# Performance work log

Hardware: AMD Instinct MI355X
Metric: run time of the kernel (lower is better)

The kernel has to match this reference:

```python
import jax, jax.numpy as jnp
import numpy as np

B, M, D, H, DH = 4, 2048, 1024, 16, 64
R_ATTN, FFN_D, R_FFN = 32, 4096, 512
ROPE_THETA = 10000.0
LN_EPS = 1e-5


def layernorm(x, w, b):
    mu = jnp.mean(x, axis=-1, keepdims=True)
    var = jnp.mean(jnp.square(x - mu), axis=-1, keepdims=True)
    return (x - mu) * jax.lax.rsqrt(var + LN_EPS) * w + b


def headwise_svd(x, U, V, b):
    # x: [B,M,D]; U: [H,D,r]; V: [H,r,dh] -> [B,M,H,dh]
    xr = jnp.einsum('bmd,hdr->bmhr', x, U)
    y = jnp.einsum('bmhr,hrk->bmhk', xr, V)
    return y + b.reshape(U.shape[0], -1)


def rotate_half(x):
    x1, x2 = jnp.split(x, 2, axis=-1)
    return jnp.concatenate([-x2, x1], axis=-1)


def rope_cos_sin(m, dh, dtype):
    inv_freq = 1.0 / (ROPE_THETA ** (jnp.arange(0, dh, 2, dtype=jnp.float32) / dh))
    freqs = jnp.arange(m, dtype=jnp.float32)[:, None] * inv_freq[None, :]  # [M, dh/2]
    emb = jnp.concatenate([freqs, freqs], axis=-1)  # [M, dh]
    return jnp.cos(emb).astype(dtype), jnp.sin(emb).astype(dtype)


def setup_inputs() -> dict:
    key = jax.random.key(0)
    ks = jax.random.split(key, 16)
    s = 0.02
    def n(k, shape, scale=s):
        return jax.random.normal(k, shape, dtype=jnp.float32) * scale
    return dict(
        hidden_states=jax.random.normal(ks[0], (B, M, D), dtype=jnp.float32),
        attention_mask=jnp.ones((B, M), dtype=jnp.int32),
        ln1_w=jnp.ones((D,), jnp.float32), ln1_b=jnp.zeros((D,), jnp.float32),
        Uq=n(ks[1], (H, D, R_ATTN)), Vq=n(ks[2], (H, R_ATTN, DH)), bq=jnp.zeros((D,), jnp.float32),
        Uk=n(ks[3], (H, D, R_ATTN)), Vk=n(ks[4], (H, R_ATTN, DH)), bk=jnp.zeros((D,), jnp.float32),
        Uv=n(ks[5], (H, D, R_ATTN)), Vv=n(ks[6], (H, R_ATTN, DH)), bv=jnp.zeros((D,), jnp.float32),
        Wo_attn=n(ks[7], (D, D)), bo_attn=jnp.zeros((D,), jnp.float32),
        ln2_w=jnp.ones((D,), jnp.float32), ln2_b=jnp.zeros((D,), jnp.float32),
        U_wi=n(ks[8], (D, R_FFN)), V_wi=n(ks[9], (R_FFN, 2 * FFN_D)), b_wi=jnp.zeros((2 * FFN_D,), jnp.float32),
        U_wo=n(ks[10], (FFN_D, R_FFN)), V_wo=n(ks[11], (R_FFN, D)), b_wo=jnp.zeros((D,), jnp.float32),
    )


def reference(hidden_states, attention_mask, ln1_w, ln1_b,
              Uq, Vq, bq, Uk, Vk, bk, Uv, Vv, bv,
              Wo_attn, bo_attn, ln2_w, ln2_b,
              U_wi, V_wi, b_wi, U_wo, V_wo, b_wo):
    x = hidden_states
    xn = layernorm(x, ln1_w, ln1_b)

    # head-wise low-rank SVD QKV projections -> [B,H,M,dh]
    q = headwise_svd(xn, Uq, Vq, bq).transpose(0, 2, 1, 3)
    k = headwise_svd(xn, Uk, Vk, bk).transpose(0, 2, 1, 3)
    v = headwise_svd(xn, Uv, Vv, bv).transpose(0, 2, 1, 3)

    cos, sin = rope_cos_sin(x.shape[1], q.shape[-1], q.dtype)  # [M, dh], broadcasts
    q = q * cos + rotate_half(q) * sin
    k = k * cos + rotate_half(k) * sin

    scale = 1.0 / jnp.sqrt(jnp.asarray(q.shape[-1], q.dtype))
    scores = jnp.einsum('bhqd,bhkd->bhqk', q, k) * scale
    pad = (attention_mask == 0)[:, None, None, :]  # [B,1,1,M]
    scores = jnp.where(pad, jnp.finfo(scores.dtype).min, scores)
    attn = jax.nn.softmax(scores, axis=-1)
    ctx = jnp.einsum('bhqk,bhkd->bhqd', attn, v)
    ctx = ctx.transpose(0, 2, 1, 3).reshape(x.shape)  # [B,M,D]
    attn_out = jnp.einsum('bmd,ed->bme', ctx, Wo_attn) + bo_attn  # dense Wo (torch Linear)
    x = x + attn_out

    # FFN: low-rank Wi -> GEGLU(tanh) -> low-rank Wo
    xn2 = layernorm(x, ln2_w, ln2_b)
    h = (xn2 @ U_wi) @ V_wi + b_wi  # [B,M,2*FFN_D]
    h1, h2 = jnp.split(h, 2, axis=-1)
    g = jax.nn.gelu(h1, approximate=True) * h2  # GEGLU, tanh approx
    ffn_out = (g @ U_wo) @ V_wo + b_wo
    return x + ffn_out
```

## Files before the change

kernel.cpp:

```cpp
#include <hip/hip_runtime.h>
#include <cstdint>

#define DEV __device__ __forceinline__

typedef __attribute__((ext_vector_type(8))) short bf16x8;
typedef __attribute__((ext_vector_type(4))) float f32x4;
typedef __attribute__((ext_vector_type(16))) float f32x16;

#define MFMA(a,b,c) __builtin_amdgcn_mfma_f32_16x16x32_bf16((a),(b),(c),0,0,0)
#define MFMA32(a,b,c) __builtin_amdgcn_mfma_f32_32x32x16_bf16((a),(b),(c),0,0,0)

DEV unsigned short f2bf(float f) {
  union { float f; unsigned u; } v; v.f = f;
  unsigned r = v.u + 0x7fffu + ((v.u >> 16) & 1u);
  return (unsigned short)(r >> 16);
}
DEV float bf2f(unsigned short s) {
  union { unsigned u; float f; } v; v.u = ((unsigned)s) << 16; return v.f;
}
DEV float max3f(float a, float b, float c) { return fmaxf(fmaxf(a, b), c); }

DEV void gload16(const unsigned short* g, short* l) {
  __builtin_amdgcn_global_load_lds(
      (const __attribute__((address_space(1))) unsigned*)g,
      (__attribute__((address_space(3))) unsigned*)l, 16, 0, 0);
}


__global__ void k_build_ut(const float* __restrict__ Uq, const float* __restrict__ Uk,
                           const float* __restrict__ Uv, unsigned short* __restrict__ Ut) {
  __shared__ float tile[32][33];
  int s = blockIdx.y;
  int proj = s >> 4, h = s & 15;
  const float* U = (proj == 0) ? Uq : (proj == 1) ? Uk : Uv;
  const float* Us = U + (size_t)h * 1024 * 32;
  int d0 = blockIdx.x * 32;
  int tx = threadIdx.x, ty = threadIdx.y;
#pragma unroll
  for (int i = ty; i < 32; i += 8)
    tile[i][tx] = Us[(size_t)(d0 + i) * 32 + tx];
  __syncthreads();
#pragma unroll
  for (int i = ty; i < 32; i += 8)
    Ut[(size_t)(s * 32 + i) * 1024 + d0 + tx] = f2bf(tile[tx][i]);
}

__global__ void k_build_vt(const float* __restrict__ Vq, const float* __restrict__ Vk,
                           const float* __restrict__ Vv, unsigned short* __restrict__ Vt) {
  int ph = blockIdx.x;
  int proj = ph >> 4, h = ph & 15;
  const float* V = (proj == 0) ? Vq : (proj == 1) ? Vk : Vv;
  const float* Vs = V + (size_t)h * 2048;
  int t = threadIdx.x;
#pragma unroll
  for (int idx = t; idx < 2048; idx += 256) {
    int dh = idx >> 5, r = idx & 31;
    Vt[(size_t)ph * 2048 + idx] = f2bf(Vs[r * 64 + dh]);
  }
}

__global__ void k_f2bf(const float* __restrict__ in, unsigned short* __restrict__ out, int n) {
  int i = blockIdx.x * 256 + threadIdx.x;
  if (i < n) out[i] = f2bf(in[i]);
}

__global__ void k_transpose_bf16(const float* __restrict__ in, unsigned short* __restrict__ out,
                                 int R, int C) {
  __shared__ float tile[32][33];
  int c0 = blockIdx.x * 32, r0 = blockIdx.y * 32;
  int tx = threadIdx.x, ty = threadIdx.y;
#pragma unroll
  for (int i = ty; i < 32; i += 8)
    tile[i][tx] = in[(size_t)(r0 + i) * C + c0 + tx];
  __syncthreads();
#pragma unroll
  for (int i = ty; i < 32; i += 8)
    out[(size_t)(c0 + i) * R + r0 + tx] = f2bf(tile[tx][i]);
}

__global__ __launch_bounds__(256) void k_vtrans(const unsigned short* __restrict__ qkv,
                                                unsigned short* __restrict__ vT) {
  __shared__ short t[64][66];
  int bh = blockIdx.y, b = bh >> 4, h = bh & 15;
  int m0 = blockIdx.x << 6;
  int tid = threadIdx.x;
  int rr = tid >> 2, cc = (tid & 3) << 4;
  const unsigned short* src = qkv + ((size_t)(b * 2048 + m0 + rr)) * 3072 + 2048 + h * 64 + cc;
  *(bf16x8*)&t[rr][cc] = *(const bf16x8*)src;
  *(bf16x8*)&t[rr][cc + 8] = *(const bf16x8*)(src + 8);
  __syncthreads();
  unsigned short* dst = vT + ((size_t)bh * 64 + rr) * 2048 + m0 + cc;
  bf16x8 o0, o1;
#pragma unroll
  for (int j = 0; j < 8; ++j) o0[j] = t[cc + j][rr];
#pragma unroll
  for (int j = 0; j < 8; ++j) o1[j] = t[cc + 8 + j][rr];
  *(bf16x8*)dst = o0;
  *(bf16x8*)(dst + 8) = o1;
}

__global__ __launch_bounds__(256) void k_layernorm(const float* __restrict__ x,
                                                   const float* __restrict__ w,
                                                   const float* __restrict__ b,
                                                   unsigned short* __restrict__ out) {
  int row = blockIdx.x;
  int tid = threadIdx.x;
  int lane = tid & 63, wid = tid >> 6;
  const float4 v = ((const float4*)(x + (size_t)row * 1024))[tid];
  float s = v.x + v.y + v.z + v.w;
  float s2 = v.x * v.x + v.y * v.y + v.z * v.z + v.w * v.w;
#pragma unroll
  for (int o = 1; o < 64; o <<= 1) { s += __shfl_xor(s, o); s2 += __shfl_xor(s2, o); }
  __shared__ float as_[4], as2_[4];
  if (lane == 0) { as_[wid] = s; as2_[wid] = s2; }
  __syncthreads();
  s = as_[0] + as_[1] + as_[2] + as_[3];
  s2 = as2_[0] + as2_[1] + as2_[2] + as2_[3];
  float mean = s * (1.f / 1024.f);
  float var = s2 * (1.f / 1024.f) - mean * mean;
  float inv = rsqrtf(var + 1e-5f);
  const float4 wv = ((const float4*)w)[tid];
  const float4 bv = ((const float4*)b)[tid];
  union { unsigned short u[4]; unsigned long long ll; } o;
  o.u[0] = f2bf((v.x - mean) * inv * wv.x + bv.x);
  o.u[1] = f2bf((v.y - mean) * inv * wv.y + bv.y);
  o.u[2] = f2bf((v.z - mean) * inv * wv.z + bv.z);
  o.u[3] = f2bf((v.w - mean) * inv * wv.w + bv.w);
  ((unsigned long long*)(out + (size_t)row * 1024))[tid] = o.ll;
}

template <int EPI>
__global__ __launch_bounds__(256, 2) void k_gemm(const unsigned short* __restrict__ A,
                                                 const unsigned short* __restrict__ Bt,
                                                 const float* __restrict__ bias,
                                                 const float* __restrict__ resid,
                                                 void* __restrict__ outp, int N, int K) {
  __shared__ short Al[128 * 32];
  __shared__ short Bl[128 * 32];
  int tid = threadIdx.x, lane = tid & 63, wid = tid >> 6;
  int wr = wid >> 1, wc = wid & 1;
  size_t row0 = (size_t)blockIdx.y * 128;
  int col0 = blockIdx.x * 128;
  int arow = lane >> 2, acol = (lane & 3) << 3;
  const unsigned short* Ag = A + (row0 + wid * 32 + arow) * K + acol;
  const unsigned short* Bg = Bt + ((size_t)(col0 + wid * 32 + arow)) * K + acol;
  short* Ald = Al + wid * 1024;
  short* Bld = Bl + wid * 1024;
  f32x4 acc[4][4] = {};
  int fr = lane & 15, fk = (lane >> 4) << 3;
  for (int k0 = 0; k0 < K; k0 += 32) {
    __syncthreads();
    gload16(Ag + k0, Ald);
    gload16(Ag + (size_t)16 * K + k0, Ald + 512);
    gload16(Bg + k0, Bld);
    gload16(Bg + (size_t)16 * K + k0, Bld + 512);
    __syncthreads();
    bf16x8 af[4], bfr[4];
#pragma unroll
    for (int i = 0; i < 4; ++i) {
      af[i] = *(const bf16x8*)&Al[(wr * 64 + i * 16 + fr) * 32 + fk];
      bfr[i] = *(const bf16x8*)&Bl[(wc * 64 + i * 16 + fr) * 32 + fk];
    }
#pragma unroll
    for (int i = 0; i < 4; ++i)
#pragma unroll
      for (int j = 0; j < 4; ++j) acc[i][j] = MFMA(af[i], bfr[j], acc[i][j]);
  }
  int cr = (lane >> 4) << 2, cc = lane & 15;
#pragma unroll
  for (int j = 0; j < 4; ++j) {
    int col = col0 + wc * 64 + j * 16 + cc;
    float bb = (EPI >= 1) ? bias[col] : 0.f;
#pragma unroll
    for (int i = 0; i < 4; ++i) {
#pragma unroll
      for (int r = 0; r < 4; ++r) {
        size_t row = row0 + wr * 64 + i * 16 + cr + r;
        float v = acc[i][j][r] + bb;
        if (EPI == 2)
          ((float*)outp)[row * N + col] = v + resid[row * N + col];
        else
          ((unsigned short*)outp)[row * N + col] = f2bf(v);
      }
    }
  }
}

__global__ __launch_bounds__(256, 2) void k_qkv(const unsigned short* __restrict__ A,
                                                const unsigned short* __restrict__ Ut,
                                                const unsigned short* __restrict__ Vt,
                                                const float* __restrict__ bq,
                                                const float* __restrict__ bk,
                                                const float* __restrict__ bv,
                                                unsigned short* __restrict__ qkv) {
  __shared__ short Al[128 * 32];
  __shared__ short Bl[128 * 32];
  __shared__ short Xr[4][64 * 72];
  const int K = 1024, N3 = 3072;
  int tid = threadIdx.x, lane = tid & 63, wid = tid >> 6;
  int wr = wid >> 1, wc = wid & 1;
  size_t row0 = (size_t)blockIdx.y * 128;
  int col0 = blockIdx.x * 128;
  int arow = lane >> 2, acol = (lane & 3) << 3;
  const unsigned short* Ag = A + (row0 + wid * 32 + arow) * K + acol;
  const unsigned short* Bg = Ut + ((size_t)(col0 + wid * 32 + arow)) * K + acol;
  short* Ald = Al + wid * 1024;
  short* Bld = Bl + wid * 1024;
  f32x4 acc[4][4] = {};
  int fr = lane & 15, fk = (lane >> 4) << 3;
  for (int k0 = 0; k0 < K; k0 += 32) {
    __syncthreads();
    gload16(Ag + k0, Ald);
    gload16(Ag + (size_t)16 * K + k0, Ald + 512);
    gload16(Bg + k0, Bld);
    gload16(Bg + (size_t)16 * K + k0, Bld + 512);
    __syncthreads();
    bf16x8 af[4], bfr[4];
#pragma unroll
    for (int i = 0; i < 4; ++i) {
      af[i] = *(const bf16x8*)&Al[(wr * 64 + i * 16 + fr) * 32 + fk];
      bfr[i] = *(const bf16x8*)&Bl[(wc * 64 + i * 16 + fr) * 32 + fk];
    }
#pragma unroll
    for (int i = 0; i < 4; ++i)
#pragma unroll
      for (int j = 0; j < 4; ++j) acc[i][j] = MFMA(af[i], bfr[j], acc[i][j]);
  }
  int cr = (lane >> 4) << 2, cc = lane & 15;
  short* xw = &Xr[wid][0];
#pragma unroll
  for (int j = 0; j < 4; ++j)
#pragma unroll
    for (int i = 0; i < 4; ++i)
#pragma unroll
      for (int r = 0; r < 4; ++r)
        xw[(i * 16 + cr + r) * 72 + j * 16 + cc] = (short)f2bf(acc[i][j][r]);
  int phbase = blockIdx.x * 4 + wc * 2;
  const f32x4 zero4 = {0.f, 0.f, 0.f, 0.f};
#pragma unroll
  for (int h2 = 0; h2 < 2; ++h2) {
    int ph = phbase + h2;
    int proj = ph >> 4, hh = ph & 15;
    bf16x8 af2[4], bf2[4];
#pragma unroll
    for (int i2 = 0; i2 < 4; ++i2)
      af2[i2] = *(const bf16x8*)&xw[(i2 * 16 + fr) * 72 + h2 * 32 + fk];
#pragma unroll
    for (int j2 = 0; j2 < 4; ++j2)
      bf2[j2] = *(const bf16x8*)(Vt + ((size_t)ph * 64 + j2 * 16 + fr) * 32 + fk);
    f32x4 a2[4][4];
#pragma unroll
    for (int i2 = 0; i2 < 4; ++i2)
#pragma unroll
      for (int j2 = 0; j2 < 4; ++j2) a2[i2][j2] = MFMA(af2[i2], bf2[j2], zero4);
    const float* bp = (proj == 0) ? bq : (proj == 1) ? bk : bv;
    int obase = proj * 1024 + hh * 64;
    if (proj == 2) {
#pragma unroll
      for (int j2 = 0; j2 < 4; ++j2) {
        int dh = j2 * 16 + cc;
        float bb = bp[hh * 64 + dh];
#pragma unroll
        for (int i2 = 0; i2 < 4; ++i2)
#pragma unroll
          for (int r = 0; r < 4; ++r) {
            size_t row = row0 + wr * 64 + i2 * 16 + cr + r;
            qkv[row * N3 + obase + dh] = f2bf(a2[i2][j2][r] + bb);
          }
      }
    } else {
      float sc = (proj == 0) ? 0.18033688011112042f : 1.f;
#pragma unroll
      for (int j2 = 0; j2 < 2; ++j2) {
        int irot = j2 * 16 + cc;
        float freq = __expf((float)irot * -0.28782313662425575f);
        float bb1 = bp[hh * 64 + irot];
        float bb2 = bp[hh * 64 + irot + 32];
#pragma unroll
        for (int i2 = 0; i2 < 4; ++i2)
#pragma unroll
          for (int r = 0; r < 4; ++r) {
            size_t row = row0 + wr * 64 + i2 * 16 + cr + r;
            int m = (int)(row & 2047);
            float x1v = a2[i2][j2][r] + bb1;
            float x2v = a2[i2][j2 + 2][r] + bb2;
            float sn, csn;
            __sincosf((float)m * freq, &sn, &csn);
            qkv[row * N3 + obase + irot] = f2bf((x1v * csn - x2v * sn) * sc);
            qkv[row * N3 + obase + irot + 32] = f2bf((x2v * csn + x1v * sn) * sc);
          }
      }
    }
  }
}

__global__ __launch_bounds__(256, 2) void k_gemm_geglu(const unsigned short* __restrict__ A,
                                                       const unsigned short* __restrict__ Bt,
                                                       const float* __restrict__ bias,
                                                       unsigned short* __restrict__ out) {
  __shared__ short Al[128 * 32];
  __shared__ short B1l[128 * 32];
  __shared__ short B2l[128 * 32];
  const int K = 512;
  int tid = threadIdx.x, lane = tid & 63, wid = tid >> 6;
  int wr = wid >> 1, wc = wid & 1;
  size_t row0 = (size_t)blockIdx.y * 128;
  int col0 = blockIdx.x * 128;
  int arow = lane >> 2, acol = (lane & 3) << 3;
  const unsigned short* Ag = A + (row0 + wid * 32 + arow) * K + acol;
  const unsigned short* B1g = Bt + ((size_t)(col0 + wid * 32 + arow)) * K + acol;
  const unsigned short* B2g = Bt + ((size_t)(col0 + 4096 + wid * 32 + arow)) * K + acol;
  short* Ald = Al + wid * 1024;
  short* B1d = B1l + wid * 1024;
  short* B2d = B2l + wid * 1024;
  f32x4 acc1[4][4] = {}, acc2[4][4] = {};
  int fr = lane & 15, fk = (lane >> 4) << 3;
  for (int k0 = 0; k0 < K; k0 += 32) {
    __syncthreads();
    gload16(Ag + k0, Ald);
    gload16(Ag + (size_t)16 * K + k0, Ald + 512);
    gload16(B1g + k0, B1d);
    gload16(B1g + (size_t)16 * K + k0, B1d + 512);
    gload16(B2g + k0, B2d);
    gload16(B2g + (size_t)16 * K + k0, B2d + 512);
    __syncthreads();
    bf16x8 af[4], b1f[4], b2f[4];
#pragma unroll
    for (int i = 0; i < 4; ++i) {
      af[i] = *(const bf16x8*)&Al[(wr * 64 + i * 16 + fr) * 32 + fk];
      b1f[i] = *(const bf16x8*)&B1l[(wc * 64 + i * 16 + fr) * 32 + fk];
      b2f[i] = *(const bf16x8*)&B2l[(wc * 64 + i * 16 + fr) * 32 + fk];
    }
#pragma unroll
    for (int i = 0; i < 4; ++i)
#pragma unroll
      for (int j = 0; j < 4; ++j) {
        acc1[i][j] = MFMA(af[i], b1f[j], acc1[i][j]);
        acc2[i][j] = MFMA(af[i], b2f[j], acc2[i][j]);
      }
  }
  int cr = (lane >> 4) << 2, cc = lane & 15;
#pragma unroll
  for (int j = 0; j < 4; ++j) {
    int col = col0 + wc * 64 + j * 16 + cc;
    float bb1 = bias[col], bb2 = bias[col + 4096];
#pragma unroll
    for (int i = 0; i < 4; ++i) {
#pragma unroll
      for (int r = 0; r < 4; ++r) {
        size_t row = row0 + wr * 64 + i * 16 + cr + r;
        float h1 = acc1[i][j][r] + bb1;
        float h2 = acc2[i][j][r] + bb2;
        float u = 0.7978845608028654f * (h1 + 0.044715f * h1 * h1 * h1);
        float e = __expf(2.f * u);
        float th = 1.f - 2.f / (e + 1.f);
        float gv = 0.5f * h1 * (1.f + th) * h2;
        out[row * 4096 + col] = f2bf(gv);
      }
    }
  }
}

#define KIX(r, c) ((r) * 64 + ((c) ^ (((r) & 7) << 3)))

__global__ __launch_bounds__(256, 4) void k_attn(const unsigned short* __restrict__ qkv,
                                                 const unsigned short* __restrict__ vT,
                                                 const int* __restrict__ mask,
                                                 unsigned short* __restrict__ ctx) {
  __shared__ short Kl[64 * 64];
  __shared__ short Vl[64 * 64];
  __shared__ short Ol[4][32 * 64];
  __shared__ float mpen[64];
  __shared__ int mflag;
  int bh = blockIdx.y, b = bh >> 4, h = bh & 15;
  int q0 = blockIdx.x << 7;
  int tid = threadIdx.x, lane = tid & 63, wid = tid >> 6;
  int qi = lane & 31, hi = lane >> 5;
  const unsigned short* qrow =
      qkv + ((size_t)(b * 2048 + q0 + wid * 32 + qi)) * 3072 + h * 64 + hi * 8;
  bf16x8 qa[4];
#pragma unroll
  for (int c = 0; c < 4; ++c) qa[c] = *(const bf16x8*)(qrow + c * 16);
  float m_r = -1e30f, l_r = 0.f;
  f32x16 oacc0 = {}, oacc1 = {};
  int srw = lane >> 3;
  int schx = ((lane & 7) ^ srw) << 3;
  int rb = wid * 16;
  const unsigned short* kgb =
      qkv + ((size_t)(b * 2048 + rb + srw)) * 3072 + 1024 + h * 64 + schx;
  const unsigned short* vgb = vT + ((size_t)(bh * 64 + rb + srw)) * 2048 + schx;
  short* kld = Kl + rb * 64;
  short* vld = Vl + rb * 64;
  const int* mbase = mask + b * 2048;
  const f32x16 zero16 = {};
  int mv = (tid < 64) ? mbase[tid] : 1;
  for (int k0 = 0; k0 < 2048; k0 += 64) {
    __syncthreads();
    gload16(kgb + (size_t)k0 * 3072, kld);
    gload16(kgb + (size_t)(k0 + 8) * 3072, kld + 512);
    gload16(vgb + k0, vld);
    gload16(vgb + (size_t)8 * 2048 + k0, vld + 512);
    if (wid == 0) {
      mpen[lane] = (mv == 0) ? -1e30f : 0.f;
      unsigned long long bal = __ballot(mv == 0);
      if (lane == 0) mflag = (bal != 0ull) ? 1 : 0;
    }
    if (k0 + 64 < 2048) mv = (tid < 64) ? mbase[k0 + 64 + tid] : 1;
    __syncthreads();
#pragma unroll
    for (int kt = 0; kt < 2; ++kt) {
      f32x16 s = zero16;
      __builtin_amdgcn_s_setprio(1);
#pragma unroll
      for (int c = 0; c < 4; ++c) {
        bf16x8 kf = *(const bf16x8*)&Kl[KIX(kt * 32 + qi, c * 16 + hi * 8)];
        s = MFMA32(kf, qa[c], s);
      }
      __builtin_amdgcn_s_setprio(0);
      if (mflag) {
        const f32x4* mp4 = (const f32x4*)mpen;
#pragma unroll
        for (int t = 0; t < 4; ++t) {
          f32x4 pen = mp4[kt * 8 + t * 2 + hi];
#pragma unroll
          for (int r = 0; r < 4; ++r) s[t * 4 + r] += pen[r];
        }
      }
      float t0 = max3f(s[0], s[1], s[2]);
      float t1 = max3f(s[3], s[4], s[5]);
      float t2 = max3f(s[6], s[7], s[8]);
      float t3 = max3f(s[9], s[10], s[11]);
      float t4 = max3f(s[12], s[13], s[14]);
      float t5 = fmaxf(t0, s[15]);
      float pmax = max3f(max3f(t5, t1, t2), t3, t4);
      pmax = fmaxf(pmax, __shfl_xor(pmax, 32));
      if (!__all(pmax - m_r <= 8.f)) {
        float mn = fmaxf(m_r, pmax);
        float fac = exp2f(m_r - mn);
        m_r = mn;
        l_r *= fac;
#pragma unroll
        for (int r = 0; r < 16; ++r) { oacc0[r] *= fac; oacc1[r] *= fac; }
      }
#pragma unroll
      for (int r = 0; r < 16; ++r) s[r] = exp2f(s[r] - m_r);
      float su0 = (s[0] + s[1]) + (s[2] + s[3]);
      float su1 = (s[4] + s[5]) + (s[6] + s[7]);
      float su2 = (s[8] + s[9]) + (s[10] + s[11]);
      float su3 = (s[12] + s[13]) + (s[14] + s[15]);
      l_r += (su0 + su1) + (su2 + su3);
      unsigned pk[8];
#pragma unroll
      for (int w = 0; w < 8; ++w)
        asm("v_cvt_pk_bf16_f32 %0, %1, %2" : "=v"(pk[w]) : "v"(s[2 * w]), "v"(s[2 * w + 1]));
      unsigned a0 = pk[0], b0 = pk[2];
      unsigned a1 = pk[1], b1 = pk[3];
      unsigned a2 = pk[4], b2 = pk[6];
      unsigned a3 = pk[5], b3 = pk[7];
      asm("v_permlane32_swap_b32 %0, %1" : "+v"(a0), "+v"(b0));
      asm("v_permlane32_swap_b32 %0, %1" : "+v"(a1), "+v"(b1));
      asm("v_permlane32_swap_b32 %0, %1" : "+v"(a2), "+v"(b2));
      asm("v_permlane32_swap_b32 %0, %1" : "+v"(a3), "+v"(b3));
      union { unsigned u[4]; bf16x8 v; } pb0, pb1;
      pb0.u[0] = a0; pb0.u[1] = a1; pb0.u[2] = b0; pb0.u[3] = b1;
      pb1.u[0] = a2; pb1.u[1] = a3; pb1.u[2] = b2; pb1.u[3] = b3;
      __builtin_amdgcn_s_setprio(1);
      {
        bf16x8 vf00 = *(const bf16x8*)&Vl[KIX(qi, kt * 32 + hi * 8)];
        bf16x8 vf01 = *(const bf16x8*)&Vl[KIX(qi, kt * 32 + 16 + hi * 8)];
        oacc0 = MFMA32(vf00, pb0.v, oacc0);
        oacc0 = MFMA32(vf01, pb1.v, oacc0);
        bf16x8 vf10 = *(const bf16x8*)&Vl[KIX(32 + qi, kt * 32 + hi * 8)];
        bf16x8 vf11 = *(const bf16x8*)&Vl[KIX(32 + qi, kt * 32 + 16 + hi * 8)];
        oacc1 = MFMA32(vf10, pb0.v, oacc1);
        oacc1 = MFMA32(vf11, pb1.v, oacc1);
      }
      __builtin_amdgcn_s_setprio(0);
    }
  }
  l_r += __shfl_xor(l_r, 32);
  float invl = 1.f / l_r;
  short* ob = &Ol[wid][0];
  int xsw = (qi & 7) << 3;
#pragma unroll
  for (int t = 0; t < 4; ++t) {
    int d = t * 8 + 4 * hi;
    float a0 = oacc0[4 * t] * invl, a1 = oacc0[4 * t + 1] * invl;
    float a2 = oacc0[4 * t + 2] * invl, a3 = oacc0[4 * t + 3] * invl;
    unsigned w0, w1;
    asm("v_cvt_pk_bf16_f32 %0, %1, %2" : "=v"(w0) : "v"(a0), "v"(a1));
    asm("v_cvt_pk_bf16_f32 %0, %1, %2" : "=v"(w1) : "v"(a2), "v"(a3));
    *(unsigned long long*)&ob[qi * 64 + (d ^ xsw)] =
        ((unsigned long long)w1 << 32) | (unsigned long long)w0;
    float c0 = oacc1[4 * t] * invl, c1 = oacc1[4 * t + 1] * invl;
    float c2 = oacc1[4 * t + 2] * invl, c3 = oacc1[4 * t + 3] * invl;
    unsigned w2, w3;
    asm("v_cvt_pk_bf16_f32 %0, %1, %2" : "=v"(w2) : "v"(c0), "v"(c1));
    asm("v_cvt_pk_bf16_f32 %0, %1, %2" : "=v"(w3) : "v"(c2), "v"(c3));
    *(unsigned long long*)&ob[qi * 64 + ((d + 32) ^ xsw)] =
        ((unsigned long long)w3 << 32) | (unsigned long long)w2;
  }
  __syncthreads();
#pragma unroll
  for (int p = 0; p < 2; ++p) {
    int q = p * 16 + (lane >> 2);
    int qx = (q & 7) << 3;
    unsigned short* dst =
        ctx + ((size_t)(b * 2048 + q0 + wid * 32 + q)) * 1024 + h * 64;
#pragma unroll
    for (int j = 0; j < 2; ++j) {
      int c = (lane & 3) * 8 + j * 32;
      bf16x8 vv = *(const bf16x8*)&ob[q * 64 + (c ^ qx)];
      __builtin_nontemporal_store(vv, (bf16x8*)(dst + c));
    }
  }
}

extern "C" void kernel_launch(void* const* d_in, const int* in_sizes, int n_in, void* d_out,
                              int out_size, void* d_ws, size_t ws_size, hipStream_t stream) {
  const float* x = (const float*)d_in[0];
  const int* amask = (const int*)d_in[1];
  const float* ln1w = (const float*)d_in[2];
  const float* ln1b = (const float*)d_in[3];
  const float* Uq = (const float*)d_in[4];
  const float* Vq = (const float*)d_in[5];
  const float* bq = (const float*)d_in[6];
  const float* Uk = (const float*)d_in[7];
  const float* Vk = (const float*)d_in[8];
  const float* bk = (const float*)d_in[9];
  const float* Uv = (const float*)d_in[10];
  const float* Vv = (const float*)d_in[11];
  const float* bv = (const float*)d_in[12];
  const float* Wo = (const float*)d_in[13];
  const float* bo = (const float*)d_in[14];
  const float* ln2w = (const float*)d_in[15];
  const float* ln2b = (const float*)d_in[16];
  const float* Uwi = (const float*)d_in[17];
  const float* Vwi = (const float*)d_in[18];
  const float* bwi = (const float*)d_in[19];
  const float* Uwo = (const float*)d_in[20];
  const float* Vwo = (const float*)d_in[21];
  const float* bwo = (const float*)d_in[22];

  char* ws = (char*)d_ws;
  size_t off = 0;
  auto alloc = [&](size_t bytes) {
    void* p = ws + off;
    off += (bytes + 255) & ~(size_t)255;
    return p;
  };
  unsigned short* xn = (unsigned short*)alloc((size_t)8192 * 1024 * 2);
  unsigned short* Ut = (unsigned short*)alloc((size_t)1536 * 1024 * 2);
  unsigned short* Vt = (unsigned short*)alloc((size_t)48 * 2048 * 2);
  unsigned short* Wob = (unsigned short*)alloc((size_t)1024 * 1024 * 2);
  unsigned short* Uwit = (unsigned short*)alloc((size_t)512 * 1024 * 2);
  unsigned short* Vwit = (unsigned short*)alloc((size_t)8192 * 512 * 2);
  unsigned short* Uwot = (unsigned short*)alloc((size_t)512 * 4096 * 2);
  unsigned short* Vwot = (unsigned short*)alloc((size_t)1024 * 512 * 2);
  unsigned short* qkv = (unsigned short*)alloc((size_t)8192 * 3072 * 2);
  unsigned short* ctx = (unsigned short*)alloc((size_t)8192 * 1024 * 2);
  float* x1 = (float*)alloc((size_t)8192 * 1024 * 4);
  unsigned short* hr = (unsigned short*)alloc((size_t)8192 * 512 * 2);
  unsigned short* gr = (unsigned short*)alloc((size_t)8192 * 512 * 2);
  unsigned short* g = qkv;
  unsigned short* xn2 = xn;
  unsigned short* vT = (unsigned short*)x1;
  if (off > ws_size) return;
  (void)in_sizes; (void)n_in; (void)out_size;

  dim3 tb(32, 8);
  k_build_ut<<<dim3(32, 48), tb, 0, stream>>>(Uq, Uk, Uv, Ut);
  k_build_vt<<<48, 256, 0, stream>>>(Vq, Vk, Vv, Vt);
  k_f2bf<<<4096, 256, 0, stream>>>(Wo, Wob, 1024 * 1024);
  k_transpose_bf16<<<dim3(512 / 32, 1024 / 32), tb, 0, stream>>>(Uwi, Uwit, 1024, 512);
  k_transpose_bf16<<<dim3(8192 / 32, 512 / 32), tb, 0, stream>>>(Vwi, Vwit, 512, 8192);
  k_transpose_bf16<<<dim3(512 / 32, 4096 / 32), tb, 0, stream>>>(Uwo, Uwot, 4096, 512);
  k_transpose_bf16<<<dim3(1024 / 32, 512 / 32), tb, 0, stream>>>(Vwo, Vwot, 512, 1024);

  k_layernorm<<<8192, 256, 0, stream>>>(x, ln1w, ln1b, xn);
  k_qkv<<<dim3(12, 64), 256, 0, stream>>>(xn, Ut, Vt, bq, bk, bv, qkv);
  k_vtrans<<<dim3(32, 64), 256, 0, stream>>>(qkv, vT);
  k_attn<<<dim3(16, 64), 256, 0, stream>>>(qkv, vT, amask, ctx);
  k_gemm<2><<<dim3(8, 64), 256, 0, stream>>>(ctx, Wob, bo, x, x1, 1024, 1024);
  k_layernorm<<<8192, 256, 0, stream>>>(x1, ln2w, ln2b, xn2);
  k_gemm<0><<<dim3(4, 64), 256, 0, stream>>>(xn2, Uwit, nullptr, nullptr, hr, 512, 1024);
  k_gemm_geglu<<<dim3(32, 64), 256, 0, stream>>>(hr, Vwit, bwi, g);
  k_gemm<0><<<dim3(4, 64), 256, 0, stream>>>(g, Uwot, nullptr, nullptr, gr, 512, 4096);
  k_gemm<2><<<dim3(8, 64), 256, 0, stream>>>(gr, Vwot, bwo, x1, d_out, 1024, 512);
}
```

Baseline: 485.7 us.

## Fuse V transpose into QKV epilogue, double GEMM K-tile, row-per-wave layernorm

Removes the separate V-transpose kernel by writing V directly in transposed layout from the QKV projection epilogue. Doubles the K-step of all GEMM kernels to 64, halving barrier and loop overhead at the cost of more shared memory. Layernorm now handles one row per wave, which drops the cross-wave shared-memory reduction and barrier. The wider LDS rows may introduce bank conflicts and lower occupancy.

```diff
diff --git a/kernel.cpp b/kernel.cpp
--- a/kernel.cpp
+++ b/kernel.cpp
@@ -78,55 +78,38 @@
     out[(size_t)(c0 + i) * R + r0 + tx] = f2bf(tile[tx][i]);
 }
 
-__global__ __launch_bounds__(256) void k_vtrans(const unsigned short* __restrict__ qkv,
-                                                unsigned short* __restrict__ vT) {
-  __shared__ short t[64][66];
-  int bh = blockIdx.y, b = bh >> 4, h = bh & 15;
-  int m0 = blockIdx.x << 6;
-  int tid = threadIdx.x;
-  int rr = tid >> 2, cc = (tid & 3) << 4;
-  const unsigned short* src = qkv + ((size_t)(b * 2048 + m0 + rr)) * 3072 + 2048 + h * 64 + cc;
-  *(bf16x8*)&t[rr][cc] = *(const bf16x8*)src;
-  *(bf16x8*)&t[rr][cc + 8] = *(const bf16x8*)(src + 8);
-  __syncthreads();
-  unsigned short* dst = vT + ((size_t)bh * 64 + rr) * 2048 + m0 + cc;
-  bf16x8 o0, o1;
-#pragma unroll
-  for (int j = 0; j < 8; ++j) o0[j] = t[cc + j][rr];
-#pragma unroll
-  for (int j = 0; j < 8; ++j) o1[j] = t[cc + 8 + j][rr];
-  *(bf16x8*)dst = o0;
-  *(bf16x8*)(dst + 8) = o1;
-}
-
 __global__ __launch_bounds__(256) void k_layernorm(const float* __restrict__ x,
                                                    const float* __restrict__ w,
                                                    const float* __restrict__ b,
                                                    unsigned short* __restrict__ out) {
-  int row = blockIdx.x;
-  int tid = threadIdx.x;
-  int lane = tid & 63, wid = tid >> 6;
-  const float4 v = ((const float4*)(x + (size_t)row * 1024))[tid];
-  float s = v.x + v.y + v.z + v.w;
-  float s2 = v.x * v.x + v.y * v.y + v.z * v.z + v.w * v.w;
+  int lane = threadIdx.x & 63, wid = threadIdx.x >> 6;
+  size_t row = (size_t)blockIdx.x * 4 + wid;
+  const float4* xr = (const float4*)(x + row * 1024);
+  float4 v[4];
+  float s = 0.f, s2 = 0.f;
+#pragma unroll
+  for (int t = 0; t < 4; ++t) {
+    v[t] = xr[lane + t * 64];
+    s += v[t].x + v[t].y + v[t].z + v[t].w;
+    s2 += v[t].x * v[t].x + v[t].y * v[t].y + v[t].z * v[t].z + v[t].w * v[t].w;
+  }
 #pragma unroll
   for (int o = 1; o < 64; o <<= 1) { s += __shfl_xor(s, o); s2 += __shfl_xor(s2, o); }
-  __shared__ float as_[4], as2_[4];
-  if (lane == 0) { as_[wid] = s; as2_[wid] = s2; }
-  __syncthreads();
-  s = as_[0] + as_[1] + as_[2] + as_[3];
-  s2 = as2_[0] + as2_[1] + as2_[2] + as2_[3];
   float mean = s * (1.f / 1024.f);
   float var = s2 * (1.f / 1024.f) - mean * mean;
   float inv = rsqrtf(var + 1e-5f);
-  const float4 wv = ((const float4*)w)[tid];
-  const float4 bv = ((const float4*)b)[tid];
-  union { unsigned short u[4]; unsigned long long ll; } o;
-  o.u[0] = f2bf((v.x - mean) * inv * wv.x + bv.x);
-  o.u[1] = f2bf((v.y - mean) * inv * wv.y + bv.y);
-  o.u[2] = f2bf((v.z - mean) * inv * wv.z + bv.z);
-  o.u[3] = f2bf((v.w - mean) * inv * wv.w + bv.w);
-  ((unsigned long long*)(out + (size_t)row * 1024))[tid] = o.ll;
+  unsigned long long* op = (unsigned long long*)(out + row * 1024);
+#pragma unroll
+  for (int t = 0; t < 4; ++t) {
+    float4 wv = ((const float4*)w)[lane + t * 64];
+    float4 bv = ((const float4*)b)[lane + t * 64];
+    union { unsigned short u[4]; unsigned long long ll; } o;
+    o.u[0] = f2bf((v[t].x - mean) * inv * wv.x + bv.x);
+    o.u[1] = f2bf((v[t].y - mean) * inv * wv.y + bv.y);
+    o.u[2] = f2bf((v[t].z - mean) * inv * wv.z + bv.z);
+    o.u[3] = f2bf((v[t].w - mean) * inv * wv.w + bv.w);
+    op[lane + t * 64] = o.ll;
+  }
 }
 
 template <int EPI>
@@ -135,36 +118,43 @@
                                                  const float* __restrict__ bias,
                                                  const float* __restrict__ resid,
                                                  void* __restrict__ outp, int N, int K) {
-  __shared__ short Al[128 * 32];
-  __shared__ short Bl[128 * 32];
+  __shared__ short Al[128 * 64];
+  __shared__ short Bl[128 * 64];
   int tid = threadIdx.x, lane = tid & 63, wid = tid >> 6;
   int wr = wid >> 1, wc = wid & 1;
   size_t row0 = (size_t)blockIdx.y * 128;
   int col0 = blockIdx.x * 128;
-  int arow = lane >> 2, acol = (lane & 3) << 3;
+  int arow = lane >> 3, acol = (lane & 7) << 3;
   const unsigned short* Ag = A + (row0 + wid * 32 + arow) * K + acol;
   const unsigned short* Bg = Bt + ((size_t)(col0 + wid * 32 + arow)) * K + acol;
-  short* Ald = Al + wid * 1024;
-  short* Bld = Bl + wid * 1024;
+  short* Ald = Al + wid * 2048;
+  short* Bld = Bl + wid * 2048;
   f32x4 acc[4][4] = {};
   int fr = lane & 15, fk = (lane >> 4) << 3;
-  for (int k0 = 0; k0 < K; k0 += 32) {
+  for (int k0 = 0; k0 < K; k0 += 64) {
     __syncthreads();
     gload16(Ag + k0, Ald);
-    gload16(Ag + (size_t)16 * K + k0, Ald + 512);
+    gload16(Ag + (size_t)8 * K + k0, Ald + 512);
+    gload16(Ag + (size_t)16 * K + k0, Ald + 1024);
+    gload16(Ag + (size_t)24 * K + k0, Ald + 1536);
     gload16(Bg + k0, Bld);
-    gload16(Bg + (size_t)16 * K + k0, Bld + 512);
-    __syncthreads();
-    bf16x8 af[4], bfr[4];
-#pragma unroll
-    for (int i = 0; i < 4; ++i) {
-      af[i] = *(const bf16x8*)&Al[(wr * 64 + i * 16 + fr) * 32 + fk];
-      bfr[i] = *(const bf16x8*)&Bl[(wc * 64 + i * 16 + fr) * 32 + fk];
-    }
-#pragma unroll
-    for (int i = 0; i < 4; ++i)
-#pragma unroll
-      for (int j = 0; j < 4; ++j) acc[i][j] = MFMA(af[i], bfr[j], acc[i][j]);
+    gload16(Bg + (size_t)8 * K + k0, Bld + 512);
+    gload16(Bg + (size_t)16 * K + k0, Bld + 1024);
+    gload16(Bg + (size_t)24 * K + k0, Bld + 1536);
+    __syncthreads();
+#pragma unroll
+    for (int hf = 0; hf < 2; ++hf) {
+      bf16x8 af[4], bfr[4];
+#pragma unroll
+      for (int i = 0; i < 4; ++i) {
+        af[i] = *(const bf16x8*)&Al[(wr * 64 + i * 16 + fr) * 64 + hf * 32 + fk];
+        bfr[i] = *(const bf16x8*)&Bl[(wc * 64 + i * 16 + fr) * 64 + hf * 32 + fk];
+      }
+#pragma unroll
+      for (int i = 0; i < 4; ++i)
+#pragma unroll
+        for (int j = 0; j < 4; ++j) acc[i][j] = MFMA(af[i], bfr[j], acc[i][j]);
+    }
   }
   int cr = (lane >> 4) << 2, cc = lane & 15;
 #pragma unroll
@@ -192,39 +182,47 @@
                                                 const float* __restrict__ bq,
                                                 const float* __restrict__ bk,
                                                 const float* __restrict__ bv,
-                                                unsigned short* __restrict__ qkv) {
-  __shared__ short Al[128 * 32];
-  __shared__ short Bl[128 * 32];
+                                                unsigned short* __restrict__ qkv,
+                                                unsigned short* __restrict__ vT) {
+  __shared__ short Al[128 * 64];
+  __shared__ short Bl[128 * 64];
   __shared__ short Xr[4][64 * 72];
   const int K = 1024, N3 = 3072;
   int tid = threadIdx.x, lane = tid & 63, wid = tid >> 6;
   int wr = wid >> 1, wc = wid & 1;
   size_t row0 = (size_t)blockIdx.y * 128;
   int col0 = blockIdx.x * 128;
-  int arow = lane >> 2, acol = (lane & 3) << 3;
+  int arow = lane >> 3, acol = (lane & 7) << 3;
   const unsigned short* Ag = A + (row0 + wid * 32 + arow) * K + acol;
   const unsigned short* Bg = Ut + ((size_t)(col0 + wid * 32 + arow)) * K + acol;
-  short* Ald = Al + wid * 1024;
-  short* Bld = Bl + wid * 1024;
+  short* Ald = Al + wid * 2048;
+  short* Bld = Bl + wid * 2048;
   f32x4 acc[4][4] = {};
   int fr = lane & 15, fk = (lane >> 4) << 3;
-  for (int k0 = 0; k0 < K; k0 += 32) {
+  for (int k0 = 0; k0 < K; k0 += 64) {
     __syncthreads();
     gload16(Ag + k0, Ald);
-    gload16(Ag + (size_t)16 * K + k0, Ald + 512);
+    gload16(Ag + (size_t)8 * K + k0, Ald + 512);
+    gload16(Ag + (size_t)16 * K + k0, Ald + 1024);
+    gload16(Ag + (size_t)24 * K + k0, Ald + 1536);
     gload16(Bg + k0, Bld);
-    gload16(Bg + (size_t)16 * K + k0, Bld + 512);
-    __syncthreads();
-    bf16x8 af[4], bfr[4];
-#pragma unroll
-    for (int i = 0; i < 4; ++i) {
-      af[i] = *(const bf16x8*)&Al[(wr * 64 + i * 16 + fr) * 32 + fk];
-      bfr[i] = *(const bf16x8*)&Bl[(wc * 64 + i * 16 + fr) * 32 + fk];
-    }
-#pragma unroll
-    for (int i = 0; i < 4; ++i)
-#pragma unroll
-      for (int j = 0; j < 4; ++j) acc[i][j] = MFMA(af[i], bfr[j], acc[i][j]);
+    gload16(Bg + (size_t)8 * K + k0, Bld + 512);
+    gload16(Bg + (size_t)16 * K + k0, Bld + 1024);
+    gload16(Bg + (size_t)24 * K + k0, Bld + 1536);
+    __syncthreads();
+#pragma unroll
+    for (int hf = 0; hf < 2; ++hf) {
+      bf16x8 af[4], bfr[4];
+#pragma unroll
+      for (int i = 0; i < 4; ++i) {
+        af[i] = *(const bf16x8*)&Al[(wr * 64 + i * 16 + fr) * 64 + hf * 32 + fk];
+        bfr[i] = *(const bf16x8*)&Bl[(wc * 64 + i * 16 + fr) * 64 + hf * 32 + fk];
+      }
+#pragma unroll
+      for (int i = 0; i < 4; ++i)
+#pragma unroll
+        for (int j = 0; j < 4; ++j) acc[i][j] = MFMA(af[i], bfr[j], acc[i][j]);
+    }
   }
   int cr = (lane >> 4) << 2, cc = lane & 15;
   short* xw = &Xr[wid][0];
@@ -254,21 +252,25 @@
 #pragma unroll
       for (int j2 = 0; j2 < 4; ++j2) a2[i2][j2] = MFMA(af2[i2], bf2[j2], zero4);
     const float* bp = (proj == 0) ? bq : (proj == 1) ? bk : bv;
-    int obase = proj * 1024 + hh * 64;
     if (proj == 2) {
+      int bq_ = (int)(row0 >> 11);
+      int tok0 = (int)(row0 & 2047) + wr * 64;
+      unsigned short* vtb = vT + ((size_t)(bq_ * 16 + hh) * 64) * 2048;
 #pragma unroll
       for (int j2 = 0; j2 < 4; ++j2) {
         int dh = j2 * 16 + cc;
         float bb = bp[hh * 64 + dh];
-#pragma unroll
-        for (int i2 = 0; i2 < 4; ++i2)
-#pragma unroll
-          for (int r = 0; r < 4; ++r) {
-            size_t row = row0 + wr * 64 + i2 * 16 + cr + r;
-            qkv[row * N3 + obase + dh] = f2bf(a2[i2][j2][r] + bb);
-          }
+        unsigned short* vrow = vtb + (size_t)dh * 2048;
+#pragma unroll
+        for (int i2 = 0; i2 < 4; ++i2) {
+          union { unsigned short u[4]; unsigned long long ll; } o;
+#pragma unroll
+          for (int r = 0; r < 4; ++r) o.u[r] = f2bf(a2[i2][j2][r] + bb);
+          *(unsigned long long*)(vrow + tok0 + i2 * 16 + cr) = o.ll;
+        }
       }
     } else {
+      int obase = proj * 1024 + hh * 64;
       float sc = (proj == 0) ? 0.18033688011112042f : 1.f;
 #pragma unroll
       for (int j2 = 0; j2 < 2; ++j2) {
@@ -298,46 +300,55 @@
                                                        const unsigned short* __restrict__ Bt,
                                                        const float* __restrict__ bias,
                                                        unsigned short* __restrict__ out) {
-  __shared__ short Al[128 * 32];
-  __shared__ short B1l[128 * 32];
-  __shared__ short B2l[128 * 32];
+  __shared__ short Al[128 * 64];
+  __shared__ short B1l[128 * 64];
+  __shared__ short B2l[128 * 64];
   const int K = 512;
   int tid = threadIdx.x, lane = tid & 63, wid = tid >> 6;
   int wr = wid >> 1, wc = wid & 1;
   size_t row0 = (size_t)blockIdx.y * 128;
   int col0 = blockIdx.x * 128;
-  int arow = lane >> 2, acol = (lane & 3) << 3;
+  int arow = lane >> 3, acol = (lane & 7) << 3;
   const unsigned short* Ag = A + (row0 + wid * 32 + arow) * K + acol;
   const unsigned short* B1g = Bt + ((size_t)(col0 + wid * 32 + arow)) * K + acol;
   const unsigned short* B2g = Bt + ((size_t)(col0 + 4096 + wid * 32 + arow)) * K + acol;
-  short* Ald = Al + wid * 1024;
-  short* B1d = B1l + wid * 1024;
-  short* B2d = B2l + wid * 1024;
+  short* Ald = Al + wid * 2048;
+  short* B1d = B1l + wid * 2048;
+  short* B2d = B2l + wid * 2048;
   f32x4 acc1[4][4] = {}, acc2[4][4] = {};
   int fr = lane & 15, fk = (lane >> 4) << 3;
-  for (int k0 = 0; k0 < K; k0 += 32) {
+  for (int k0 = 0; k0 < K; k0 += 64) {
     __syncthreads();
     gload16(Ag + k0, Ald);
-    gload16(Ag + (size_t)16 * K + k0, Ald + 512);
+    gload16(Ag + (size_t)8 * K + k0, Ald + 512);
+    gload16(Ag + (size_t)16 * K + k0, Ald + 1024);
+    gload16(Ag + (size_t)24 * K + k0, Ald + 1536);
     gload16(B1g + k0, B1d);
-    gload16(B1g + (size_t)16 * K + k0, B1d + 512);
+    gload16(B1g + (size_t)8 * K + k0, B1d + 512);
+    gload16(B1g + (size_t)16 * K + k0, B1d + 1024);
+    gload16(B1g + (size_t)24 * K + k0, B1d + 1536);
     gload16(B2g + k0, B2d);
-    gload16(B2g + (size_t)16 * K + k0, B2d + 512);
-    __syncthreads();
-    bf16x8 af[4], b1f[4], b2f[4];
-#pragma unroll
-    for (int i = 0; i < 4; ++i) {
-      af[i] = *(const bf16x8*)&Al[(wr * 64 + i * 16 + fr) * 32 + fk];
-      b1f[i] = *(const bf16x8*)&B1l[(wc * 64 + i * 16 + fr) * 32 + fk];
-      b2f[i] = *(const bf16x8*)&B2l[(wc * 64 + i * 16 + fr) * 32 + fk];
-    }
-#pragma unroll
-    for (int i = 0; i < 4; ++i)
-#pragma unroll
-      for (int j = 0; j < 4; ++j) {
-        acc1[i][j] = MFMA(af[i], b1f[j], acc1[i][j]);
-        acc2[i][j] = MFMA(af[i], b2f[j], acc2[i][j]);
-      }
+    gload16(B2g + (size_t)8 * K + k0, B2d + 512);
+    gload16(B2g + (size_t)16 * K + k0, B2d + 1024);
+    gload16(B2g + (size_t)24 * K + k0, B2d + 1536);
+    __syncthreads();
+#pragma unroll
+    for (int hf = 0; hf < 2; ++hf) {
+      bf16x8 af[4], b1f[4], b2f[4];
+#pragma unroll
+      for (int i = 0; i < 4; ++i) {
+        af[i] = *(const bf16x8*)&Al[(wr * 64 + i * 16 + fr) * 64 + hf * 32 + fk];
+        b1f[i] = *(const bf16x8*)&B1l[(wc * 64 + i * 16 + fr) * 64 + hf * 32 + fk];
+        b2f[i] = *(const bf16x8*)&B2l[(wc * 64 + i * 16 + fr) * 64 + hf * 32 + fk];
+      }
+#pragma unroll
+      for (int i = 0; i < 4; ++i)
+#pragma unroll
+        for (int j = 0; j < 4; ++j) {
+          acc1[i][j] = MFMA(af[i], b1f[j], acc1[i][j]);
+          acc2[i][j] = MFMA(af[i], b2f[j], acc2[i][j]);
+        }
+    }
   }
   int cr = (lane >> 4) << 2, cc = lane & 15;
 #pragma unroll
@@ -577,12 +588,11 @@
   k_transpose_bf16<<<dim3(512 / 32, 4096 / 32), tb, 0, stream>>>(Uwo, Uwot, 4096, 512);
   k_transpose_bf16<<<dim3(1024 / 32, 512 / 32), tb, 0, stream>>>(Vwo, Vwot, 512, 1024);
 
-  k_layernorm<<<8192, 256, 0, stream>>>(x, ln1w, ln1b, xn);
-  k_qkv<<<dim3(12, 64), 256, 0, stream>>>(xn, Ut, Vt, bq, bk, bv, qkv);
-  k_vtrans<<<dim3(32, 64), 256, 0, stream>>>(qkv, vT);
+  k_layernorm<<<2048, 256, 0, stream>>>(x, ln1w, ln1b, xn);
+  k_qkv<<<dim3(12, 64), 256, 0, stream>>>(xn, Ut, Vt, bq, bk, bv, qkv, vT);
   k_attn<<<dim3(16, 64), 256, 0, stream>>>(qkv, vT, amask, ctx);
   k_gemm<2><<<dim3(8, 64), 256, 0, stream>>>(ctx, Wob, bo, x, x1, 1024, 1024);
-  k_layernorm<<<8192, 256, 0, stream>>>(x1, ln2w, ln2b, xn2);
+  k_layernorm<<<2048, 256, 0, stream>>>(x1, ln2w, ln2b, xn2);
   k_gemm<0><<<dim3(4, 64), 256, 0, stream>>>(xn2, Uwit, nullptr, nullptr, hr, 512, 1024);
   k_gemm_geglu<<<dim3(32, 64), 256, 0, stream>>>(hr, Vwit, bwi, g);
   k_gemm<0><<<dim3(4, 64), 256, 0, stream>>>(g, Uwot, nullptr, nullptr, gr, 512, 4096);
```

Result: slower. 499.4 us (+2.8%).
